# Performance work log

Measured on AMD Instinct MI355X. Metric: run time of the kernel, lower is better.

The kernel has to match this reference:

```python
import jax, jax.numpy as jnp
import numpy as np

N_NODES = 100000
N_EDGES = 1600000
EPS = 1e-5  # nn.BatchNorm1d default eps


def setup_inputs() -> dict:
    key = jax.random.key(0)
    ks = jax.random.split(key, 6)
    x = jax.random.normal(ks[0], (N_NODES, 11), dtype=jnp.float32)
    edge_index = jax.random.randint(ks[1], (2, N_EDGES), 0, N_NODES, dtype=jnp.int64)
    edge_weight = jax.random.uniform(ks[2], (N_EDGES,), dtype=jnp.float32)
    W1 = jax.random.normal(ks[3], (11, 64), dtype=jnp.float32) * 0.3
    b1 = jnp.zeros((64,), dtype=jnp.float32)
    gamma = jnp.ones((64,), dtype=jnp.float32)
    beta = jnp.zeros((64,), dtype=jnp.float32)
    W2 = jax.random.normal(ks[4], (64, 128), dtype=jnp.float32) * 0.125
    b2 = jnp.zeros((128,), dtype=jnp.float32)
    return {"x": x, "edge_index": edge_index, "edge_weight": edge_weight,
            "W1": W1, "b1": b1, "gamma": gamma, "beta": beta, "W2": W2, "b2": b2}


def _gcn_conv(x, row, col, w, W, b, n_nodes):
    """PyG GCNConv: h = x @ W; symmetric-norm aggregate at col; + bias.
    row/col/w already include self loops (weight 1.0)."""
    h = x @ W  # [N, F_out]
    deg = jax.ops.segment_sum(w, col, num_segments=n_nodes)  # [N]
    dinv = jnp.where(deg > 0, jax.lax.rsqrt(jnp.maximum(deg, 1e-12)), 0.0)
    norm = dinv[row] * w * dinv[col]  # [E+N]
    msg = h[row] * norm[:, None]  # gather + scale, [E+N, F_out]
    out = jax.ops.segment_sum(msg, col, num_segments=n_nodes)  # scatter-add
    return out + b


def _batch_norm(x, gamma, beta):
    # training-mode BatchNorm1d over node dimension, biased variance
    mean = jnp.mean(x, axis=0)
    var = jnp.mean(jnp.square(x - mean), axis=0)
    return (x - mean) * jax.lax.rsqrt(var + EPS) * gamma + beta


def reference(x, edge_index, edge_weight, W1, b1, gamma, beta, W2, b2):
    n = x.shape[0]
    loops = jnp.arange(n, dtype=edge_index.dtype)
    row = jnp.concatenate([edge_index[0], loops])
    col = jnp.concatenate([edge_index[1], loops])
    w = jnp.concatenate([edge_weight, jnp.ones((n,), dtype=edge_weight.dtype)])

    h = _gcn_conv(x, row, col, w, W1, b1, n)
    h = _batch_norm(h, gamma, beta)
    h = jax.nn.relu(h)
    # dropout is identity at inference (deterministic baseline)
    out = _gcn_conv(h, row, col, w, W2, b2, n)
    return out
```

## Files before the change

### kernel.cpp

```cpp
#include <hip/hip_runtime.h>

#define F0 11
#define F1 64
#define F2 128
#define TN2 128

#define CHUNKS 64
#define BPR 12544
#define WPR (BPR / 2)
#define NBS 1024

__device__ __forceinline__ unsigned short f2bf(float v) {
  unsigned u = __float_as_uint(v);
  unsigned r = u + 0x7FFFu + ((u >> 16) & 1u);
  return (unsigned short)(r >> 16);
}
__device__ __forceinline__ float bf2f(unsigned short s) {
  return __uint_as_float(((unsigned)s) << 16);
}

__global__ void k_pad(const float* __restrict__ x, unsigned short* __restrict__ x16b, int n) {
  int i = blockIdx.x * blockDim.x + threadIdx.x;
  if (i >= n * 16) return;
  int r = i >> 4, f = i & 15;
  x16b[i] = (f < F0) ? f2bf(x[(size_t)r * F0 + f]) : (unsigned short)0;
}

__global__ __launch_bounds__(1024) void k_hist(const int* __restrict__ col,
                                               unsigned* __restrict__ partial,
                                               int E, int CE, int N, int ranges) {
  __shared__ unsigned lds[WPR];
  int r = blockIdx.x % ranges;
  int c = blockIdx.x / ranges;
  int lo = r * BPR;
  int hi = min(N, lo + BPR);
  int t = threadIdx.x;
  for (int i = t; i < WPR; i += 1024) lds[i] = 0;
  __syncthreads();
  int e0 = c * CE, e1 = min(E, e0 + CE);
  for (int e = e0 + t; e < e1; e += 1024) {
    int b = col[e];
    if (b >= lo && b < hi) {
      int local = b - lo;
      atomicAdd(&lds[local >> 1], 1u << (16 * (local & 1)));
    }
  }
  __syncthreads();
  unsigned* dst = partial + ((size_t)r * CHUNKS + c) * WPR;
  for (int i = t; i < WPR; i += 1024) dst[i] = lds[i];
}

__global__ void k_colprefix(const unsigned* __restrict__ partial,
                            unsigned short* __restrict__ rel,
                            int* __restrict__ cnt, int N, int npad) {
  int bin = blockIdx.x * blockDim.x + threadIdx.x;
  if (bin >= N) return;
  int r = bin / BPR, local = bin % BPR;
  int word = local >> 1, sh = 16 * (local & 1);
  const unsigned* p = partial + (size_t)r * CHUNKS * WPR + word;
  unsigned acc = 0;
  for (int c = 0; c < CHUNKS; c++) {
    unsigned v = (p[(size_t)c * WPR] >> sh) & 0xFFFFu;
    rel[(size_t)c * npad + bin] = (unsigned short)acc;
    acc += v;
  }
  cnt[bin] = (int)acc;
}

__global__ void k_scan1(const int* __restrict__ cnt, int* __restrict__ offs,
                        int* __restrict__ bsum, int n) {
  __shared__ int s[1024];
  int tid = threadIdx.x;
  int i = blockIdx.x * 1024 + tid;
  int v = (i < n) ? cnt[i] : 0;
  s[tid] = v;
  __syncthreads();
  for (int d = 1; d < 1024; d <<= 1) {
    int t = (tid >= d) ? s[tid - d] : 0;
    __syncthreads();
    s[tid] += t;
    __syncthreads();
  }
  if (i < n) offs[i] = s[tid] - v;
  if (tid == 1023) bsum[blockIdx.x] = s[1023];
}

__global__ void k_scan2(int* __restrict__ bsum, int nb) {
  __shared__ int s[256];
  __shared__ int carry;
  int t = threadIdx.x;
  if (t == 0) carry = 0;
  __syncthreads();
  for (int base = 0; base < nb; base += 256) {
    int v = (base + t < nb) ? bsum[base + t] : 0;
    s[t] = v;
    __syncthreads();
    for (int d = 1; d < 256; d <<= 1) {
      int x = (t >= d) ? s[t - d] : 0;
      __syncthreads();
      s[t] += x;
      __syncthreads();
    }
    int total = s[255];
    if (base + t < nb) bsum[base + t] = carry + s[t] - v;
    __syncthreads();
    if (t == 0) carry += total;
    __syncthreads();
  }
}

__global__ void k_scan3(int* __restrict__ offs, const int* __restrict__ bsum,
                        int n, int total) {
  int i = blockIdx.x * 1024 + threadIdx.x;
  if (i < n) offs[i] += bsum[blockIdx.x];
  if (i == 0) offs[n] = total;
}

__global__ __launch_bounds__(1024) void k_fill(const int* __restrict__ row,
                                               const int* __restrict__ col,
                                               const float* __restrict__ w,
                                               const int* __restrict__ offs,
                                               const unsigned short* __restrict__ rel,
                                               uint2* __restrict__ csr8,
                                               int E, int CE, int N, int npad, int ranges) {
  __shared__ unsigned cur[WPR];
  int r = blockIdx.x % ranges;
  int c = blockIdx.x / ranges;
  int lo = r * BPR;
  int hi = min(N, lo + BPR);
  int t = threadIdx.x;
  const unsigned* rsrc = (const unsigned*)(rel + (size_t)c * npad + lo);
  int nw = (hi - lo + 1) >> 1;
  for (int i = t; i < nw; i += 1024) cur[i] = rsrc[i];
  __syncthreads();
  int e0 = c * CE, e1 = min(E, e0 + CE);
  for (int e = e0 + t; e < e1; e += 1024) {
    int b = col[e];
    if (b >= lo && b < hi) {
      int local = b - lo;
      int sh = 16 * (local & 1);
      unsigned old = atomicAdd(&cur[local >> 1], 1u << sh);
      unsigned myrel = (old >> sh) & 0xFFFFu;
      int pos = offs[b] + (int)myrel;
      csr8[pos] = make_uint2((unsigned)row[e], __float_as_uint(w[e]));
    }
  }
}

__global__ void k_deg2(const uint2* __restrict__ csr8, const int* __restrict__ offs,
                       float* __restrict__ dinv, int n) {
  int wid = (blockIdx.x * blockDim.x + threadIdx.x) >> 6;
  int lane = threadIdx.x & 63;
  if (wid >= n) return;
  int s = offs[wid], e = offs[wid + 1];
  float acc = 0.f;
  for (int k = s + lane; k < e; k += 64) acc += __uint_as_float(csr8[k].y);
#pragma unroll
  for (int d = 32; d > 0; d >>= 1) acc += __shfl_down(acc, d);
  if (lane == 0) dinv[wid] = rsqrtf(1.0f + acc);
}

__global__ void k_agg1g(const unsigned short* __restrict__ x16b, const int* __restrict__ offs,
                        const uint2* __restrict__ csr8, const float* __restrict__ dinv,
                        const float* __restrict__ W1, const float* __restrict__ b1,
                        unsigned short* __restrict__ h, int n) {
  __shared__ float Ws[F0 * F1];
  __shared__ float bs[F1];
  __shared__ unsigned s_soff[4][64];
  __shared__ float    s_nrm[4][64];
  int t = threadIdx.x;
  for (int i = t; i < F0 * F1; i += 256) Ws[i] = W1[i];
  if (t < F1) bs[t] = b1[t];
  __syncthreads();
  int wv = t >> 6;
  int lane = t & 63;
  int wid = (blockIdx.x * blockDim.x + t) >> 6;
  if (wid >= n) return;
  int g = lane >> 4, f = lane & 15;
  float di = dinv[wid];
  float acc0 = (g == 0) ? di * bf2f(x16b[(size_t)wid * 16 + f]) : 0.f;
  float acc1 = 0.f;
  int s = offs[wid], e = offs[wid + 1];
  for (int base = s; base < e; base += 64) {
    int m = e - base; if (m > 64) m = 64;
    if (lane < m) {
      uint2 v = csr8[base + lane];
      s_soff[wv][lane] = v.x * 16u;
      s_nrm[wv][lane] = dinv[v.x] * __uint_as_float(v.y);
    }
    for (int j = 0; j < m; j += 8) {
      int j0 = j + g, j1 = j + 4 + g;
      unsigned o0 = (j0 < m) ? s_soff[wv][j0] : 0u;
      float    m0 = (j0 < m) ? s_nrm[wv][j0] : 0.f;
      unsigned o1 = (j1 < m) ? s_soff[wv][j1] : 0u;
      float    m1 = (j1 < m) ? s_nrm[wv][j1] : 0.f;
      acc0 += m0 * bf2f(x16b[(size_t)o0 + f]);
      acc1 += m1 * bf2f(x16b[(size_t)o1 + f]);
    }
  }
  float acc = acc0 + acc1;
  acc += __shfl_xor(acc, 16);
  acc += __shfl_xor(acc, 32);
  float av = di * acc;
  float o = bs[lane];
#pragma unroll
  for (int k = 0; k < F0; k++) o += __shfl(av, k) * Ws[k * F1 + lane];
  h[(size_t)wid * F1 + lane] = f2bf(o);
}

__global__ void k_bn_stats(const unsigned short* __restrict__ h, float2* __restrict__ pbn,
                           int total) {
  int t = threadIdx.x;
  int idx = blockIdx.x * blockDim.x + t;
  int stride = gridDim.x * blockDim.x;
  float s = 0.0f, q = 0.0f;
  for (int i = idx; i < total; i += stride) {
    float v = bf2f(h[i]);
    s += v; q += v * v;
  }
  __shared__ float ss[256], qq[256];
  ss[t] = s; qq[t] = q;
  __syncthreads();
  if (t < 64) {
    float S = ss[t] + ss[t + 64] + ss[t + 128] + ss[t + 192];
    float Q = qq[t] + qq[t + 64] + qq[t + 128] + qq[t + 192];
    pbn[(size_t)blockIdx.x * 64 + t] = make_float2(S, Q);
  }
}

__global__ void k_bn_mid(const float2* __restrict__ pbn, float2* __restrict__ pbn2) {
  __shared__ float sS[4][64], sQ[4][64];
  int t = threadIdx.x;
  int f = t & 63, g = t >> 6;
  int b0 = blockIdx.x * 16;
  float S = 0.f, Q = 0.f;
  for (int b = b0 + g; b < b0 + 16; b += 4) {
    float2 v = pbn[(size_t)b * 64 + f];
    S += v.x; Q += v.y;
  }
  sS[g][f] = S; sQ[g][f] = Q;
  __syncthreads();
  if (t < 64)
    pbn2[(size_t)blockIdx.x * 64 + t] =
        make_float2(sS[0][t] + sS[1][t] + sS[2][t] + sS[3][t],
                    sQ[0][t] + sQ[1][t] + sQ[2][t] + sQ[3][t]);
}

__global__ void k_bn_final(const float2* __restrict__ pbn2, const float* __restrict__ gamma,
                           const float* __restrict__ beta, float* __restrict__ scalef,
                           float* __restrict__ shiftf, int n) {
  __shared__ double sS[4][64], sQ[4][64];
  int t = threadIdx.x;
  int f = t & 63, g = t >> 6;
  double S = 0.0, Q = 0.0;
  for (int b = g; b < 64; b += 4) {
    float2 v = pbn2[(size_t)b * 64 + f];
    S += v.x; Q += v.y;
  }
  sS[g][f] = S; sQ[g][f] = Q;
  __syncthreads();
  if (t < 64) {
    double SS = sS[0][t] + sS[1][t] + sS[2][t] + sS[3][t];
    double QQ = sQ[0][t] + sQ[1][t] + sQ[2][t] + sQ[3][t];
    double mean = SS / (double)n;
    double var = QQ / (double)n - mean * mean;
    if (var < 0.0) var = 0.0;
    float scale = gamma[t] * (float)(1.0 / sqrt(var + 1e-5));
    scalef[t] = scale;
    shiftf[t] = beta[t] - (float)mean * scale;
  }
}

__global__ void k_agg2(const unsigned short* __restrict__ h, const int* __restrict__ offs,
                       const uint2* __restrict__ csr8, const float* __restrict__ dinv,
                       const float* __restrict__ scalef, const float* __restrict__ shiftf,
                       float* __restrict__ agg2, int n) {
  __shared__ unsigned s_soff[4][64];
  __shared__ float    s_nrm[4][64];
  int t = threadIdx.x;
  int wv = t >> 6;
  int lane = t & 63;
  int wid = (blockIdx.x * blockDim.x + t) >> 6;
  if (wid >= n) return;
  float sc = scalef[lane], sf = shiftf[lane];
  float di = dinv[wid];
  float a0 = di * fmaxf(fmaf(bf2f(h[(size_t)wid * F1 + lane]), sc, sf), 0.f);
  float a1 = 0.f, a2 = 0.f, a3 = 0.f;
  int s = offs[wid], e = offs[wid + 1];
  for (int base = s; base < e; base += 64) {
    int m = e - base; if (m > 64) m = 64;
    if (lane < m) {
      uint2 v = csr8[base + lane];
      s_soff[wv][lane] = v.x * 64u;
      s_nrm[wv][lane] = dinv[v.x] * __uint_as_float(v.y);
    }
    int j = 0;
    for (; j + 4 <= m; j += 4) {
      unsigned o0 = s_soff[wv][j + 0], o1 = s_soff[wv][j + 1];
      unsigned o2 = s_soff[wv][j + 2], o3 = s_soff[wv][j + 3];
      float m0 = s_nrm[wv][j + 0], m1 = s_nrm[wv][j + 1];
      float m2 = s_nrm[wv][j + 2], m3 = s_nrm[wv][j + 3];
      a0 += m0 * fmaxf(fmaf(bf2f(h[(size_t)o0 + lane]), sc, sf), 0.f);
      a1 += m1 * fmaxf(fmaf(bf2f(h[(size_t)o1 + lane]), sc, sf), 0.f);
      a2 += m2 * fmaxf(fmaf(bf2f(h[(size_t)o2 + lane]), sc, sf), 0.f);
      a3 += m3 * fmaxf(fmaf(bf2f(h[(size_t)o3 + lane]), sc, sf), 0.f);
    }
    for (; j < m; j++) {
      unsigned o = s_soff[wv][j];
      float nm = s_nrm[wv][j];
      a0 += nm * fmaxf(fmaf(bf2f(h[(size_t)o + lane]), sc, sf), 0.f);
    }
  }
  agg2[(size_t)wid * F1 + lane] = di * ((a0 + a1) + (a2 + a3));
}

__global__ __launch_bounds__(256) void k_gemm2(const float* __restrict__ agg2,
                                               const float* __restrict__ W2,
                                               const float* __restrict__ b2,
                                               float* __restrict__ out, int n) {
  __shared__ float Ws[F1 * F2];
  __shared__ float As[F1][TN2];
  int t = threadIdx.x;
  for (int i = t; i < F1 * F2 / 4; i += 256) ((float4*)Ws)[i] = ((const float4*)W2)[i];
  int nb = blockIdx.x * TN2;
  int node = t & 127;
  int kh = (t >> 7) * 32;
  int gnode = nb + node;
  if (gnode < n) {
    const float4* src = (const float4*)(agg2 + (size_t)gnode * F1 + kh);
#pragma unroll
    for (int j = 0; j < 8; j++) {
      float4 v = src[j];
      As[kh + j * 4 + 0][node] = v.x;
      As[kh + j * 4 + 1][node] = v.y;
      As[kh + j * 4 + 2][node] = v.z;
      As[kh + j * 4 + 3][node] = v.w;
    }
  } else {
#pragma unroll
    for (int j = 0; j < 8; j++) {
      As[kh + j * 4 + 0][node] = 0.f;
      As[kh + j * 4 + 1][node] = 0.f;
      As[kh + j * 4 + 2][node] = 0.f;
      As[kh + j * 4 + 3][node] = 0.f;
    }
  }
  __syncthreads();

  int f0 = (t & 15) * 8;
  int n0 = (t >> 4) * 8;
  float acc[8][8];
  float bv[8];
#pragma unroll
  for (int j = 0; j < 8; j++) bv[j] = b2[f0 + j];
#pragma unroll
  for (int i = 0; i < 8; i++)
#pragma unroll
    for (int j = 0; j < 8; j++) acc[i][j] = bv[j];

#pragma unroll 4
  for (int k = 0; k < F1; k++) {
    float4 a0 = *(const float4*)&As[k][n0];
    float4 a1 = *(const float4*)&As[k][n0 + 4];
    float4 w0 = *(const float4*)&Ws[k * F2 + f0];
    float4 w1 = *(const float4*)&Ws[k * F2 + f0 + 4];
    float a[8] = {a0.x, a0.y, a0.z, a0.w, a1.x, a1.y, a1.z, a1.w};
    float w[8] = {w0.x, w0.y, w0.z, w0.w, w1.x, w1.y, w1.z, w1.w};
#pragma unroll
    for (int i = 0; i < 8; i++)
#pragma unroll
      for (int j = 0; j < 8; j++) acc[i][j] += a[i] * w[j];
  }

#pragma unroll
  for (int i = 0; i < 8; i++) {
    int gi = nb + n0 + i;
    if (gi < n) {
      float4 o0 = {acc[i][0], acc[i][1], acc[i][2], acc[i][3]};
      float4 o1 = {acc[i][4], acc[i][5], acc[i][6], acc[i][7]};
      *(float4*)&out[(size_t)gi * F2 + f0] = o0;
      *(float4*)&out[(size_t)gi * F2 + f0 + 4] = o1;
    }
  }
}

extern "C" void kernel_launch(void* const* d_in, const int* in_sizes, int n_in,
                              void* d_out, int out_size, void* d_ws, size_t ws_size,
                              hipStream_t stream) {
  const float* x     = (const float*)d_in[0];
  const int*   ei    = (const int*)d_in[1];
  const float* ew    = (const float*)d_in[2];
  const float* W1    = (const float*)d_in[3];
  const float* b1    = (const float*)d_in[4];
  const float* gamma = (const float*)d_in[5];
  const float* beta  = (const float*)d_in[6];
  const float* W2    = (const float*)d_in[7];
  const float* b2    = (const float*)d_in[8];
  float* out = (float*)d_out;

  int N = in_sizes[0] / F0;
  int E = in_sizes[1] / 2;
  const int* row = ei;
  const int* col = ei + E;
  if (N <= 0) return;

  int CE = (E + CHUNKS - 1) / CHUNKS;
  int RANGES = (N + BPR - 1) / BPR;
  int npad = RANGES * BPR;

  char* p = (char*)d_ws;
  auto alloc = [&](size_t bytes) -> void* {
    void* r = (void*)p;
    p += (bytes + 255) & ~(size_t)255;
    return r;
  };
  size_t partial_bytes = ((size_t)RANGES * CHUNKS * WPR * 4 + 255) & ~(size_t)255;
  size_t rel_bytes     = (size_t)CHUNKS * npad * 2;
  size_t h_bytes       = (size_t)N * F1 * 2;
  size_t region_bytes  = partial_bytes + rel_bytes;
  if (h_bytes > region_bytes) region_bytes = h_bytes;

  float*          dinv    = (float*)alloc((size_t)N * 4);
  int*            cnt     = (int*)alloc((size_t)N * 4);
  int*            offs    = (int*)alloc((size_t)(N + 1) * 4);
  int             NB      = (N + 1023) / 1024;
  int*            bsum    = (int*)alloc((size_t)NB * 4);
  uint2*          csr8    = (uint2*)alloc((size_t)E * 8);
  char*           region  = (char*)alloc(region_bytes);
  unsigned*       partial = (unsigned*)region;
  unsigned short* rel     = (unsigned short*)(region + partial_bytes);
  unsigned short* h       = (unsigned short*)region;
  unsigned short* x16b    = (unsigned short*)alloc((size_t)N * 16 * 2);
  float*          agg2    = (float*)alloc((size_t)N * F1 * 4);
  float2*         pbn     = (float2*)alloc((size_t)NBS * 64 * 8);
  float2*         pbn2    = (float2*)alloc((size_t)64 * 64 * 8);
  float*          scalef  = (float*)alloc(64 * 4);
  float*          shiftf  = (float*)alloc(64 * 4);
  (void)ws_size; (void)n_in; (void)out_size;

  int bW = (N + 3) / 4;
  int bG2 = (N + TN2 - 1) / TN2;
  int gRC = CHUNKS * RANGES;

  k_pad<<<(N * 16 + 255) / 256, 256, 0, stream>>>(x, x16b, N);
  k_hist<<<gRC, 1024, 0, stream>>>(col, partial, E, CE, N, RANGES);
  k_colprefix<<<(N + 255) / 256, 256, 0, stream>>>(partial, rel, cnt, N, npad);
  k_scan1<<<NB, 1024, 0, stream>>>(cnt, offs, bsum, N);
  k_scan2<<<1, 256, 0, stream>>>(bsum, NB);
  k_scan3<<<NB, 1024, 0, stream>>>(offs, bsum, N, E);
  k_fill<<<gRC, 1024, 0, stream>>>(row, col, ew, offs, rel, csr8, E, CE, N, npad, RANGES);
  k_deg2<<<bW, 256, 0, stream>>>(csr8, offs, dinv, N);
  k_agg1g<<<bW, 256, 0, stream>>>(x16b, offs, csr8, dinv, W1, b1, h, N);
  k_bn_stats<<<NBS, 256, 0, stream>>>(h, pbn, N * F1);
  k_bn_mid<<<64, 256, 0, stream>>>(pbn, pbn2);
  k_bn_final<<<1, 256, 0, stream>>>(pbn2, gamma, beta, scalef, shiftf, N);
  k_agg2<<<bW, 256, 0, stream>>>(h, offs, csr8, dinv, scalef, shiftf, agg2, N);
  k_gemm2<<<bG2, 256, 0, stream>>>(agg2, W2, b2, out, N);
}
```

Before: 252.7 us.

## Precompute source-side norm into CSR, unroll gathers, vectorize BN stats

Adds a pass that multiplies each CSR edge weight by dinv of its source once, so both aggregation kernels stop doing a random dinv gather per edge. The layer-1 aggregation now handles 16 edges per iteration with four accumulators, and both aggregations zero-pad shared slots so the tail branches disappear. The BN stats kernel reads four bf16 values per load, keeping per-feature partials in a 2D shared array. The cost is an extra launch plus a read-modify-write pass over the 1.7M-entry CSR array.

```diff
diff --git a/kernel.cpp b/kernel.cpp
--- a/kernel.cpp
+++ b/kernel.cpp
@@ -17,6 +17,12 @@
 }
 __device__ __forceinline__ float bf2f(unsigned short s) {
   return __uint_as_float(((unsigned)s) << 16);
+}
+__device__ __forceinline__ float bf2f_lo(unsigned v) {
+  return __uint_as_float(v << 16);
+}
+__device__ __forceinline__ float bf2f_hi(unsigned v) {
+  return __uint_as_float(v & 0xFFFF0000u);
 }
 
 __global__ void k_pad(const float* __restrict__ x, unsigned short* __restrict__ x16b, int n) {
@@ -160,6 +166,13 @@
   if (lane == 0) dinv[wid] = rsqrtf(1.0f + acc);
 }
 
+__global__ void k_norm(uint2* __restrict__ csr8, const float* __restrict__ dinv, int E) {
+  int i = blockIdx.x * blockDim.x + threadIdx.x;
+  if (i >= E) return;
+  uint2 v = csr8[i];
+  csr8[i].y = __float_as_uint(dinv[v.x] * __uint_as_float(v.y));
+}
+
 __global__ void k_agg1g(const unsigned short* __restrict__ x16b, const int* __restrict__ offs,
                         const uint2* __restrict__ csr8, const float* __restrict__ dinv,
                         const float* __restrict__ W1, const float* __restrict__ b1,
@@ -178,27 +191,32 @@
   if (wid >= n) return;
   int g = lane >> 4, f = lane & 15;
   float di = dinv[wid];
-  float acc0 = (g == 0) ? di * bf2f(x16b[(size_t)wid * 16 + f]) : 0.f;
-  float acc1 = 0.f;
+  float a0 = (g == 0) ? di * bf2f(x16b[(size_t)wid * 16 + f]) : 0.f;
+  float a1 = 0.f, a2 = 0.f, a3 = 0.f;
   int s = offs[wid], e = offs[wid + 1];
   for (int base = s; base < e; base += 64) {
     int m = e - base; if (m > 64) m = 64;
     if (lane < m) {
       uint2 v = csr8[base + lane];
       s_soff[wv][lane] = v.x * 16u;
-      s_nrm[wv][lane] = dinv[v.x] * __uint_as_float(v.y);
-    }
-    for (int j = 0; j < m; j += 8) {
-      int j0 = j + g, j1 = j + 4 + g;
-      unsigned o0 = (j0 < m) ? s_soff[wv][j0] : 0u;
-      float    m0 = (j0 < m) ? s_nrm[wv][j0] : 0.f;
-      unsigned o1 = (j1 < m) ? s_soff[wv][j1] : 0u;
-      float    m1 = (j1 < m) ? s_nrm[wv][j1] : 0.f;
-      acc0 += m0 * bf2f(x16b[(size_t)o0 + f]);
-      acc1 += m1 * bf2f(x16b[(size_t)o1 + f]);
-    }
-  }
-  float acc = acc0 + acc1;
+      s_nrm[wv][lane] = __uint_as_float(v.y);
+    } else {
+      s_soff[wv][lane] = 0u;
+      s_nrm[wv][lane] = 0.f;
+    }
+    int mp = (m + 15) & ~15;
+    for (int jb = 0; jb < mp; jb += 16) {
+      unsigned o0 = s_soff[wv][jb + g],      o1 = s_soff[wv][jb + 4 + g];
+      unsigned o2 = s_soff[wv][jb + 8 + g],  o3 = s_soff[wv][jb + 12 + g];
+      float    m0 = s_nrm[wv][jb + g],       m1 = s_nrm[wv][jb + 4 + g];
+      float    m2 = s_nrm[wv][jb + 8 + g],   m3 = s_nrm[wv][jb + 12 + g];
+      a0 += m0 * bf2f(x16b[(size_t)o0 + f]);
+      a1 += m1 * bf2f(x16b[(size_t)o1 + f]);
+      a2 += m2 * bf2f(x16b[(size_t)o2 + f]);
+      a3 += m3 * bf2f(x16b[(size_t)o3 + f]);
+    }
+  }
+  float acc = (a0 + a1) + (a2 + a3);
   acc += __shfl_xor(acc, 16);
   acc += __shfl_xor(acc, 32);
   float av = di * acc;
@@ -209,21 +227,33 @@
 }
 
 __global__ void k_bn_stats(const unsigned short* __restrict__ h, float2* __restrict__ pbn,
-                           int total) {
+                           int total4) {
   int t = threadIdx.x;
   int idx = blockIdx.x * blockDim.x + t;
   int stride = gridDim.x * blockDim.x;
-  float s = 0.0f, q = 0.0f;
-  for (int i = idx; i < total; i += stride) {
-    float v = bf2f(h[i]);
-    s += v; q += v * v;
-  }
-  __shared__ float ss[256], qq[256];
-  ss[t] = s; qq[t] = q;
+  const uint2* hp = (const uint2*)h;
+  float s0 = 0, s1 = 0, s2 = 0, s3 = 0, q0 = 0, q1 = 0, q2 = 0, q3 = 0;
+  for (int i = idx; i < total4; i += stride) {
+    uint2 v = hp[i];
+    float a = bf2f_lo(v.x), b = bf2f_hi(v.x);
+    float c = bf2f_lo(v.y), d = bf2f_hi(v.y);
+    s0 += a; q0 += a * a;
+    s1 += b; q1 += b * b;
+    s2 += c; q2 += c * c;
+    s3 += d; q3 += d * d;
+  }
+  __shared__ float ss[256][4], qq[256][4];
+  ss[t][0] = s0; ss[t][1] = s1; ss[t][2] = s2; ss[t][3] = s3;
+  qq[t][0] = q0; qq[t][1] = q1; qq[t][2] = q2; qq[t][3] = q3;
   __syncthreads();
   if (t < 64) {
-    float S = ss[t] + ss[t + 64] + ss[t + 128] + ss[t + 192];
-    float Q = qq[t] + qq[t + 64] + qq[t + 128] + qq[t + 192];
+    int o = t >> 2, sub = t & 3;
+    float S = 0.f, Q = 0.f;
+#pragma unroll
+    for (int i = 0; i < 16; i++) {
+      S += ss[o + 16 * i][sub];
+      Q += qq[o + 16 * i][sub];
+    }
     pbn[(size_t)blockIdx.x * 64 + t] = make_float2(S, Q);
   }
 }
@@ -292,10 +322,13 @@
     if (lane < m) {
       uint2 v = csr8[base + lane];
       s_soff[wv][lane] = v.x * 64u;
-      s_nrm[wv][lane] = dinv[v.x] * __uint_as_float(v.y);
-    }
-    int j = 0;
-    for (; j + 4 <= m; j += 4) {
+      s_nrm[wv][lane] = __uint_as_float(v.y);
+    } else {
+      s_soff[wv][lane] = 0u;
+      s_nrm[wv][lane] = 0.f;
+    }
+    int mp = (m + 3) & ~3;
+    for (int j = 0; j < mp; j += 4) {
       unsigned o0 = s_soff[wv][j + 0], o1 = s_soff[wv][j + 1];
       unsigned o2 = s_soff[wv][j + 2], o3 = s_soff[wv][j + 3];
       float m0 = s_nrm[wv][j + 0], m1 = s_nrm[wv][j + 1];
@@ -304,11 +337,6 @@
       a1 += m1 * fmaxf(fmaf(bf2f(h[(size_t)o1 + lane]), sc, sf), 0.f);
       a2 += m2 * fmaxf(fmaf(bf2f(h[(size_t)o2 + lane]), sc, sf), 0.f);
       a3 += m3 * fmaxf(fmaf(bf2f(h[(size_t)o3 + lane]), sc, sf), 0.f);
-    }
-    for (; j < m; j++) {
-      unsigned o = s_soff[wv][j];
-      float nm = s_nrm[wv][j];
-      a0 += nm * fmaxf(fmaf(bf2f(h[(size_t)o + lane]), sc, sf), 0.f);
     }
   }
   agg2[(size_t)wid * F1 + lane] = di * ((a0 + a1) + (a2 + a3));
@@ -450,8 +478,9 @@
   k_scan3<<<NB, 1024, 0, stream>>>(offs, bsum, N, E);
   k_fill<<<gRC, 1024, 0, stream>>>(row, col, ew, offs, rel, csr8, E, CE, N, npad, RANGES);
   k_deg2<<<bW, 256, 0, stream>>>(csr8, offs, dinv, N);
+  k_norm<<<(E + 255) / 256, 256, 0, stream>>>(csr8, dinv, E);
   k_agg1g<<<bW, 256, 0, stream>>>(x16b, offs, csr8, dinv, W1, b1, h, N);
-  k_bn_stats<<<NBS, 256, 0, stream>>>(h, pbn, N * F1);
+  k_bn_stats<<<NBS, 256, 0, stream>>>(h, pbn, N * F1 / 4);
   k_bn_mid<<<64, 256, 0, stream>>>(pbn, pbn2);
   k_bn_final<<<1, 256, 0, stream>>>(pbn2, gamma, beta, scalef, shiftf, N);
   k_agg2<<<bW, 256, 0, stream>>>(h, offs, csr8, dinv, scalef, shiftf, agg2, N);
```

New measurement: 247.3 us. -2.1%, faster.
